# Performance work log

Hardware: AMD Instinct MI355X
Metric: run time of the kernel (lower is better)

The kernel has to match this reference:

```python
import jax, jax.numpy as jnp
import numpy as np

BS, CIN, COUT, OUT_DIM, S, S0 = 64, 128, 128, 1024, 2, 1
BLK = S * (S0 + 1)  # 4
D = OUT_DIM * BLK   # 4096


def setup_inputs() -> dict:
    key = jax.random.key(0)
    kx, kw = jax.random.split(key)
    x = jax.random.normal(kx, (BS, CIN, D), dtype=jnp.float32)
    weight = jax.random.normal(kw, (COUT, CIN, D), dtype=jnp.float32)
    return {"x": x, "weight": weight}


def reference(x, weight):
    # Equivalent to: (x[:, None] * weight).reshape(bs, cout, cin, out_dim, blk).sum((-1, -3)) / sqrt(cin)
    bs, cin, d = x.shape
    cout = weight.shape[0]
    blk = BLK
    xr = x.reshape(bs, cin, d // blk, blk)          # (bs, cin, out_dim, blk)
    wr = weight.reshape(cout, cin, d // blk, blk)   # (cout, cin, out_dim, blk)
    # Blocked locally-connected contraction over (cin, blk), fused -- never
    # materializes the (bs, cout, cin, d) broadcast intermediate.
    out = jnp.einsum('bink,oink->bon', xr, wr)
    return out / jnp.sqrt(jnp.asarray(cin, dtype=x.dtype))
```

## Files before the change

kernel.cpp:

```cpp
#include <hip/hip_runtime.h>


#define CIN    128
#define COUT   128
#define ODIM   1024
#define DDIM   4096
#define NB     4
#define CI     8
#define NCHUNK (CIN/CI)
#define LROW   36
#define XPL    (64*LROW + 2)
#define BUFS   (NB*XPL)

typedef short  bf16x8 __attribute__((ext_vector_type(8)));
typedef short  s16x4  __attribute__((ext_vector_type(4)));
typedef float  f32x4  __attribute__((ext_vector_type(4)));

static __device__ __forceinline__ unsigned short f2bf(float f) {
    unsigned int u = __float_as_uint(f);
    u += 0x7fffu + ((u >> 16) & 1u);
    return (unsigned short)(u >> 16);
}
static __device__ __forceinline__ s16x4 cvt4(float4 v) {
    s16x4 s;
    s[0] = (short)f2bf(v.x); s[1] = (short)f2bf(v.y);
    s[2] = (short)f2bf(v.z); s[3] = (short)f2bf(v.w);
    return s;
}

__global__ __launch_bounds__(512, 4)
void nolc_kernel(const float* __restrict__ xg,
                 const float* __restrict__ wg,
                 float* __restrict__ outg) {
    __shared__ short xs[2 * BUFS];
    __shared__ short ws[2 * BUFS];

    const int bid  = blockIdx.x;
    const int xcd  = bid & 7;
    const int gidx = xcd * 64 + (bid >> 3);
    const int bn   = gidx >> 1;
    const int oh   = gidx & 1;

    const int t    = threadIdx.x;
    const int lane = t & 63;
    const int wave = t >> 6;
    const int dbase = 16 * bn;

    const int sn  = t & 3;
    const int sii = (t >> 2) & 7;
    const int sr  = t >> 5;
    const size_t ITS  = (size_t)16 * CIN * DDIM;
    const size_t CSTR = (size_t)CI * DDIM;

    const float* xp = xg + (size_t)(sr * CIN + sii) * DDIM + dbase + 4 * sn;
    const float* wp = wg + ((size_t)(oh * 64 + sr) * CIN + sii) * DDIM + dbase + 4 * sn;
    const int ldso = sn * XPL + sr * LROW + sii * 4;

    const int bt  = wave & 3;
    const int ot  = wave >> 2;
    const int row = lane & 15;
    const int kg  = lane >> 4;

    f32x4 acc[2][4];
#pragma unroll
    for (int j = 0; j < 2; ++j)
#pragma unroll
        for (int n = 0; n < 4; ++n)
            acc[j][n] = (f32x4){0.f, 0.f, 0.f, 0.f};

    float4 rxA[4], rwA[4], rxB[4], rwB[4];

#define LOADC(rx, rw, c)                                                     \
    do {                                                                     \
        const float* _xp = xp + (size_t)(c) * CSTR;                          \
        const float* _wp = wp + (size_t)(c) * CSTR;                          \
        _Pragma("unroll")                                                    \
        for (int it = 0; it < 4; ++it) {                                     \
            rx[it] = *reinterpret_cast<const float4*>(_xp + it * ITS);       \
            rw[it] = *reinterpret_cast<const float4*>(_wp + it * ITS);       \
        }                                                                    \
    } while (0)

#define STAGE(rx, rw, sel)                                                   \
    do {                                                                     \
        _Pragma("unroll")                                                    \
        for (int it = 0; it < 4; ++it) {                                     \
            *reinterpret_cast<s16x4*>(&xs[(sel) * BUFS + ldso + it * 16 * LROW]) = cvt4(rx[it]); \
            *reinterpret_cast<s16x4*>(&ws[(sel) * BUFS + ldso + it * 16 * LROW]) = cvt4(rw[it]); \
        }                                                                    \
    } while (0)

#define COMPUTE(sel)                                                         \
    do {                                                                     \
        const short* _xb = &xs[(sel) * BUFS + (bt * 16 + row) * LROW + kg * 8]; \
        const short* _wb = &ws[(sel) * BUFS + (ot * 32 + row) * LROW + kg * 8]; \
        _Pragma("unroll")                                                    \
        for (int n = 0; n < 4; ++n) {                                        \
            bf16x8 a = *reinterpret_cast<const bf16x8*>(_xb + n * XPL);      \
            _Pragma("unroll")                                                \
            for (int j = 0; j < 2; ++j) {                                    \
                bf16x8 bb = *reinterpret_cast<const bf16x8*>(_wb + n * XPL + j * 16 * LROW); \
                acc[j][n] = __builtin_amdgcn_mfma_f32_16x16x32_bf16(a, bb, acc[j][n], 0, 0, 0); \
            }                                                                \
        }                                                                    \
    } while (0)

    LOADC(rxA, rwA, 0);
    for (int c = 0; c < NCHUNK; c += 2) {
        LOADC(rxB, rwB, c + 1);
        STAGE(rxA, rwA, 0);
        asm volatile("s_waitcnt lgkmcnt(0)" ::: "memory");
        __builtin_amdgcn_s_barrier();
        COMPUTE(0);

        if (c + 2 < NCHUNK) LOADC(rxA, rwA, c + 2);
        STAGE(rxB, rwB, 1);
        asm volatile("s_waitcnt lgkmcnt(0)" ::: "memory");
        __builtin_amdgcn_s_barrier();
        COMPUTE(1);
    }
#undef LOADC
#undef STAGE
#undef COMPUTE

    const float scale = 0.08838834764831845f;
#pragma unroll
    for (int j = 0; j < 2; ++j) {
        const int o = oh * 64 + ot * 32 + j * 16 + row;
#pragma unroll
        for (int r = 0; r < 4; ++r) {
            const int b = bt * 16 + kg * 4 + r;
            float4 v;
            v.x = acc[j][0][r] * scale;
            v.y = acc[j][1][r] * scale;
            v.z = acc[j][2][r] * scale;
            v.w = acc[j][3][r] * scale;
            *reinterpret_cast<float4*>(outg + ((size_t)b * COUT + o) * ODIM + 4 * bn) = v;
        }
    }
}

extern "C" void kernel_launch(void* const* d_in, const int* in_sizes, int n_in,
                              void* d_out, int out_size, void* d_ws, size_t ws_size,
                              hipStream_t stream) {
    const float* x = (const float*)d_in[0];
    const float* w = (const float*)d_in[1];
    float* out = (float*)d_out;
    nolc_kernel<<<dim3(512), dim3(512), 0, stream>>>(x, w, out);
}
```

Baseline: 163.6 us.

## Widen block tile to 8 output positions with XOR-swizzled shared layout

Each block now covers 8 output positions (32 d-elements) for 64 couts using 1024 threads, and the grid halves to 256 blocks. The padded LDS layout is replaced by 256-short rows with an XOR swizzle on 8-element pieces, meant to avoid bank conflicts on the staging writes and the MFMA operand reads. The wave tiling changes so each wave handles a 16x16 (b,o) tile across 8 positions, and outputs are written as two float4 per row. The larger blocks with 4x less... fewer blocks (256) may underfill the 256 CUs' occupancy, and launch_bounds(1024,4) limits registers.

```diff
diff --git a/kernel.cpp b/kernel.cpp
--- a/kernel.cpp
+++ b/kernel.cpp
@@ -5,12 +5,10 @@
 #define COUT   128
 #define ODIM   1024
 #define DDIM   4096
-#define NB     4
+#define NB     8
 #define CI     8
-#define NCHUNK (CIN/CI)
-#define LROW   36
-#define XPL    (64*LROW + 2)
-#define BUFS   (NB*XPL)
+#define NCH    16
+#define RS     256
 
 typedef short  bf16x8 __attribute__((ext_vector_type(8)));
 typedef short  s16x4  __attribute__((ext_vector_type(4)));
@@ -28,92 +26,90 @@
     return s;
 }
 
-__global__ __launch_bounds__(512, 4)
+__global__ __launch_bounds__(1024, 4)
 void nolc_kernel(const float* __restrict__ xg,
                  const float* __restrict__ wg,
                  float* __restrict__ outg) {
-    __shared__ short xs[2 * BUFS];
-    __shared__ short ws[2 * BUFS];
+    __shared__ short xs[2][64 * RS];
+    __shared__ short ws[2][64 * RS];
 
     const int bid  = blockIdx.x;
-    const int xcd  = bid & 7;
-    const int gidx = xcd * 64 + (bid >> 3);
-    const int bn   = gidx >> 1;
+    const int gidx = (bid & 7) * 32 + (bid >> 3);
+    const int bng  = gidx >> 1;
     const int oh   = gidx & 1;
 
     const int t    = threadIdx.x;
     const int lane = t & 63;
     const int wave = t >> 6;
-    const int dbase = 16 * bn;
+    const int bq   = wave & 3;
+    const int oq   = wave >> 2;
+    const int row  = lane & 15;
+    const int kg   = lane >> 4;
 
-    const int sn  = t & 3;
-    const int sii = (t >> 2) & 7;
-    const int sr  = t >> 5;
+    const int dbase = 32 * bng;
+
+    const int sn4  = t & 7;
+    const int sii  = (t >> 3) & 7;
+    const int srow = t >> 6;
     const size_t ITS  = (size_t)16 * CIN * DDIM;
     const size_t CSTR = (size_t)CI * DDIM;
 
-    const float* xp = xg + (size_t)(sr * CIN + sii) * DDIM + dbase + 4 * sn;
-    const float* wp = wg + ((size_t)(oh * 64 + sr) * CIN + sii) * DDIM + dbase + 4 * sn;
-    const int ldso = sn * XPL + sr * LROW + sii * 4;
+    const float* xp = xg + (size_t)(srow * CIN + sii) * DDIM + dbase + 4 * sn4;
+    const float* wp = wg + ((size_t)(oh * 64 + srow) * CIN + sii) * DDIM + dbase + 4 * sn4;
 
-    const int bt  = wave & 3;
-    const int ot  = wave >> 2;
-    const int row = lane & 15;
-    const int kg  = lane >> 4;
+    const int spiece = sn4 * 4 + (sii >> 1);
+    const int ldso = srow * RS + (((spiece ^ (srow & 7))) << 3) + (sii & 1) * 4;
 
-    f32x4 acc[2][4];
+    f32x4 acc[NB];
 #pragma unroll
-    for (int j = 0; j < 2; ++j)
-#pragma unroll
-        for (int n = 0; n < 4; ++n)
-            acc[j][n] = (f32x4){0.f, 0.f, 0.f, 0.f};
+    for (int n = 0; n < NB; ++n) acc[n] = (f32x4){0.f, 0.f, 0.f, 0.f};
 
     float4 rxA[4], rwA[4], rxB[4], rwB[4];
 
-#define LOADC(rx, rw, c)                                                     \
-    do {                                                                     \
-        const float* _xp = xp + (size_t)(c) * CSTR;                          \
-        const float* _wp = wp + (size_t)(c) * CSTR;                          \
-        _Pragma("unroll")                                                    \
-        for (int it = 0; it < 4; ++it) {                                     \
-            rx[it] = *reinterpret_cast<const float4*>(_xp + it * ITS);       \
-            rw[it] = *reinterpret_cast<const float4*>(_wp + it * ITS);       \
-        }                                                                    \
+#define LOADC(rx, rw, c)                                                      \
+    do {                                                                      \
+        const float* _xp = xp + (size_t)(c) * CSTR;                           \
+        const float* _wp = wp + (size_t)(c) * CSTR;                           \
+        _Pragma("unroll")                                                     \
+        for (int it = 0; it < 4; ++it) {                                      \
+            rx[it] = *reinterpret_cast<const float4*>(_xp + it * ITS);        \
+            rw[it] = *reinterpret_cast<const float4*>(_wp + it * ITS);        \
+        }                                                                     \
     } while (0)
 
-#define STAGE(rx, rw, sel)                                                   \
-    do {                                                                     \
-        _Pragma("unroll")                                                    \
-        for (int it = 0; it < 4; ++it) {                                     \
-            *reinterpret_cast<s16x4*>(&xs[(sel) * BUFS + ldso + it * 16 * LROW]) = cvt4(rx[it]); \
-            *reinterpret_cast<s16x4*>(&ws[(sel) * BUFS + ldso + it * 16 * LROW]) = cvt4(rw[it]); \
-        }                                                                    \
+#define STAGE(rx, rw, sel)                                                    \
+    do {                                                                      \
+        _Pragma("unroll")                                                     \
+        for (int it = 0; it < 4; ++it) {                                      \
+            *reinterpret_cast<s16x4*>(&xs[sel][ldso + it * 16 * RS]) = cvt4(rx[it]); \
+            *reinterpret_cast<s16x4*>(&ws[sel][ldso + it * 16 * RS]) = cvt4(rw[it]); \
+        }                                                                     \
     } while (0)
 
-#define COMPUTE(sel)                                                         \
-    do {                                                                     \
-        const short* _xb = &xs[(sel) * BUFS + (bt * 16 + row) * LROW + kg * 8]; \
-        const short* _wb = &ws[(sel) * BUFS + (ot * 32 + row) * LROW + kg * 8]; \
-        _Pragma("unroll")                                                    \
-        for (int n = 0; n < 4; ++n) {                                        \
-            bf16x8 a = *reinterpret_cast<const bf16x8*>(_xb + n * XPL);      \
-            _Pragma("unroll")                                                \
-            for (int j = 0; j < 2; ++j) {                                    \
-                bf16x8 bb = *reinterpret_cast<const bf16x8*>(_wb + n * XPL + j * 16 * LROW); \
-                acc[j][n] = __builtin_amdgcn_mfma_f32_16x16x32_bf16(a, bb, acc[j][n], 0, 0, 0); \
-            }                                                                \
-        }                                                                    \
+    const int xrb = (bq * 16 + row) * RS;
+    const int wrb = (oq * 16 + row) * RS;
+    const int r8  = row & 7;
+
+#define COMPUTE(sel)                                                          \
+    do {                                                                      \
+        _Pragma("unroll")                                                     \
+        for (int n = 0; n < NB; ++n) {                                        \
+            const int po = ((n * 4 + kg) ^ r8) * 8;                           \
+            bf16x8 a  = *reinterpret_cast<const bf16x8*>(&xs[sel][xrb + po]); \
+            bf16x8 bb = *reinterpret_cast<const bf16x8*>(&ws[sel][wrb + po]); \
+            acc[n] = __builtin_amdgcn_mfma_f32_16x16x32_bf16(a, bb, acc[n], 0, 0, 0); \
+        }                                                                     \
     } while (0)
 
     LOADC(rxA, rwA, 0);
-    for (int c = 0; c < NCHUNK; c += 2) {
+    for (int c = 0; c < NCH; c += 2) {
         LOADC(rxB, rwB, c + 1);
         STAGE(rxA, rwA, 0);
         asm volatile("s_waitcnt lgkmcnt(0)" ::: "memory");
         __builtin_amdgcn_s_barrier();
         COMPUTE(0);
 
-        if (c + 2 < NCHUNK) LOADC(rxA, rwA, c + 2);
+        if (c + 2 < NCH) LOADC(rxA, rwA, c + 2);
         STAGE(rxB, rwB, 1);
         asm volatile("s_waitcnt lgkmcnt(0)" ::: "memory");
         __builtin_amdgcn_s_barrier();
@@ -124,19 +120,19 @@
 #undef COMPUTE
 
     const float scale = 0.08838834764831845f;
+    const int o = oh * 64 + oq * 16 + row;
+    const int n0 = 8 * bng;
 #pragma unroll
-    for (int j = 0; j < 2; ++j) {
-        const int o = oh * 64 + ot * 32 + j * 16 + row;
-#pragma unroll
-        for (int r = 0; r < 4; ++r) {
-            const int b = bt * 16 + kg * 4 + r;
-            float4 v;
-            v.x = acc[j][0][r] * scale;
-            v.y = acc[j][1][r] * scale;
-            v.z = acc[j][2][r] * scale;
-            v.w = acc[j][3][r] * scale;
-            *reinterpret_cast<float4*>(outg + ((size_t)b * COUT + o) * ODIM + 4 * bn) = v;
-        }
+    for (int r = 0; r < 4; ++r) {
+        const int b = bq * 16 + kg * 4 + r;
+        float* op = outg + ((size_t)b * COUT + o) * ODIM + n0;
+        float4 v0, v1;
+        v0.x = acc[0][r] * scale; v0.y = acc[1][r] * scale;
+        v0.z = acc[2][r] * scale; v0.w = acc[3][r] * scale;
+        v1.x = acc[4][r] * scale; v1.y = acc[5][r] * scale;
+        v1.z = acc[6][r] * scale; v1.w = acc[7][r] * scale;
+        *reinterpret_cast<float4*>(op)     = v0;
+        *reinterpret_cast<float4*>(op + 4) = v1;
     }
 }
 
@@ -146,5 +142,5 @@
     const float* x = (const float*)d_in[0];
     const float* w = (const float*)d_in[1];
     float* out = (float*)d_out;
-    nolc_kernel<<<dim3(512), dim3(512), 0, stream>>>(x, w, out);
+    nolc_kernel<<<dim3(256), dim3(1024), 0, stream>>>(x, w, out);
 }
```

Measured after the change: 132.8 us. 1.23x faster.
